# Kernel optimization log

Measured on AMD Instinct MI355X. Metric: run time of the kernel, lower is better.

Reference implementation:

```python
import jax, jax.numpy as jnp
import numpy as np
import math

B, N, D = 4, 2048, 256
H = 8
HD = D // H  # 32
EPS = 1e-5


def _layernorm(x, gamma, beta):
    mu = jnp.mean(x, axis=-1, keepdims=True)
    var = jnp.var(x, axis=-1, keepdims=True)
    return (x - mu) * jax.lax.rsqrt(var + EPS) * gamma + beta


def setup_inputs() -> dict:
    key = jax.random.key(0)
    ks = jax.random.split(key, 16)
    s = 0.02
    inp = {
        "x": jax.random.normal(ks[0], (B, N, D), dtype=jnp.float32),
        "adj": jax.random.randint(ks[1], (B, N, N), 0, 2, dtype=jnp.int32),
        "wq": jax.random.normal(ks[2], (D, D), dtype=jnp.float32) * s,
        "bq": jnp.zeros((D,), jnp.float32),
        "wk": jax.random.normal(ks[3], (D, D), dtype=jnp.float32) * s,
        "bk": jnp.zeros((D,), jnp.float32),
        "wv": jax.random.normal(ks[4], (D, D), dtype=jnp.float32) * s,
        "bv": jnp.zeros((D,), jnp.float32),
        "wo": jax.random.normal(ks[5], (D, D), dtype=jnp.float32) * s,
        "bo": jnp.zeros((D,), jnp.float32),
        "g1": jnp.ones((D,), jnp.float32),
        "be1": jnp.zeros((D,), jnp.float32),
        "g2": jnp.ones((D,), jnp.float32),
        "be2": jnp.zeros((D,), jnp.float32),
        "w1": jax.random.normal(ks[6], (D, 4 * D), dtype=jnp.float32) * s,
        "b1": jnp.zeros((4 * D,), jnp.float32),
        "w2": jax.random.normal(ks[7], (4 * D, D), dtype=jnp.float32) * s,
        "b2": jnp.zeros((D,), jnp.float32),
    }
    return inp


def reference(x, adj, wq, bq, wk, bk, wv, bv, wo, bo, g1, be1, g2, be2, w1, b1, w2, b2):
    # Dropout is identity in eval mode.
    res = x
    xn = _layernorm(x, g1, be1)
    q = (xn @ wq + bq).reshape(B, N, H, HD).transpose(0, 2, 1, 3)  # (B,H,N,d)
    k = (xn @ wk + bk).reshape(B, N, H, HD).transpose(0, 2, 1, 3)
    v = (xn @ wv + bv).reshape(B, N, H, HD).transpose(0, 2, 1, 3)
    scores = jnp.einsum("bhnd,bhmd->bhnm", q, k) / math.sqrt(HD)
    scores = jnp.where(adj[:, None, :, :] == 0, -jnp.inf, scores)
    attn = jax.nn.softmax(scores, axis=-1)
    attn = jnp.nan_to_num(attn, nan=0.0)  # rows with no edges -> all zeros
    out = jnp.einsum("bhnm,bhmd->bhnd", attn, v)
    out = out.transpose(0, 2, 1, 3).reshape(B, N, D)
    out = out @ wo + bo
    x = res + out
    h = _layernorm(x, g2, be2)
    h = jax.nn.gelu(h @ w1 + b1, approximate=False) @ w2 + b2
    return x + h
```

## Files before the change

### kernel.cpp

```cpp
#include <hip/hip_runtime.h>
#include <hip/hip_bf16.h>
#include <math.h>

#define B_ 4
#define N_ 2048
#define D_ 256
#define H_ 8
#define HD_ 32
#define F_ 1024
#define M_ (B_*N_)
#define EPS_ 1e-5f
#define VSTR 72

typedef __attribute__((ext_vector_type(8))) short short8;
typedef __attribute__((ext_vector_type(4))) float f32x4;

#define QSC 0.2550565499f

#if __has_builtin(__builtin_amdgcn_exp2f)
__device__ inline float fexp2(float x) { return __builtin_amdgcn_exp2f(x); }
#else
__device__ inline float fexp2(float x) { float r; asm("v_exp_f32 %0, %1" : "=v"(r) : "v"(x)); return r; }
#endif
#if __has_builtin(__builtin_amdgcn_rcpf)
__device__ inline float frcp(float x) { return __builtin_amdgcn_rcpf(x); }
#else
__device__ inline float frcp(float x) { float r; asm("v_rcp_f32 %0, %1" : "=v"(r) : "v"(x)); return r; }
#endif

__device__ inline unsigned short f2bf(float f) {
    union { float f; unsigned u; } x; x.f = f;
    unsigned r = x.u + 0x7fff + ((x.u >> 16) & 1);
    return (unsigned short)(r >> 16);
}

__device__ inline unsigned pk_bf16(float a, float b) {
    union { __hip_bfloat162 h; unsigned u; } c;
    c.h = __float22bfloat162_rn(float2{a, b});
    return c.u;
}

__device__ inline float gelu_f(float x) {
    float ax = fabsf(x);
    float z = ax * 0.70710678118654752f;
    float t = frcp(fmaf(0.3275911f, z, 1.0f));
    float e = fexp2(-z * z * 1.4426950408889634f);
    float poly = t * fmaf(t, fmaf(t, fmaf(t, fmaf(t, 1.061405429f, -1.453152027f),
                     1.421413741f), -0.284496736f), 0.254829592f);
    float erfv = 1.0f - poly * e;
    float s = (x < 0.f) ? -erfv : erfv;
    return 0.5f * x * (1.0f + s);
}

__device__ inline void async_copy16(const void* g, void* l) {
    __builtin_amdgcn_global_load_lds(
        (const __attribute__((address_space(1))) void*)g,
        (__attribute__((address_space(3))) void*)l, 16, 0, 0);
}

__device__ inline void ln_rows(const float* __restrict__ x,
        const float* __restrict__ g, const float* __restrict__ be,
        unsigned short* __restrict__ out, int blk) {
    int w = threadIdx.x >> 6, lane = threadIdx.x & 63;
    int row = blk * 4 + w;
    float4 v = *(const float4*)&x[(size_t)row * D_ + lane * 4];
    float s  = v.x + v.y + v.z + v.w;
    float s2 = v.x * v.x + v.y * v.y + v.z * v.z + v.w * v.w;
    #pragma unroll
    for (int off = 1; off < 64; off <<= 1) {
        s  += __shfl_xor(s,  off, 64);
        s2 += __shfl_xor(s2, off, 64);
    }
    float mu  = s * (1.0f / D_);
    float var = s2 * (1.0f / D_) - mu * mu;
    float r = rsqrtf(var + EPS_);
    float4 gv = *(const float4*)&g[lane * 4];
    float4 bv = *(const float4*)&be[lane * 4];
    ushort4 u;
    u.x = f2bf((v.x - mu) * r * gv.x + bv.x);
    u.y = f2bf((v.y - mu) * r * gv.y + bv.y);
    u.z = f2bf((v.z - mu) * r * gv.z + bv.z);
    u.w = f2bf((v.w - mu) * r * gv.w + bv.w);
    *(ushort4*)&out[(size_t)row * D_ + lane * 4] = u;
}

__global__ __launch_bounds__(256) void ln_kernel(const float* __restrict__ x,
        const float* __restrict__ g, const float* __restrict__ be,
        unsigned short* __restrict__ out) {
    ln_rows(x, g, be, out, blockIdx.x);
}

__global__ __launch_bounds__(256) void prep_kernel(
        const int* __restrict__ adj, unsigned short* __restrict__ mask16,
        const float* __restrict__ wq, const float* __restrict__ wk,
        const float* __restrict__ wv, const float* __restrict__ wo,
        const float* __restrict__ w1, const float* __restrict__ w2,
        unsigned short* __restrict__ wqkvt, unsigned short* __restrict__ wot,
        unsigned short* __restrict__ w1t, unsigned short* __restrict__ w2t,
        const float* __restrict__ x, const float* __restrict__ g1,
        const float* __restrict__ be1, unsigned short* __restrict__ xn) {
    __shared__ float t[32][33];
    int id = blockIdx.x;
    if (id < 4096) {
        int g = id * 256 + threadIdx.x;
        const int4* ap = (const int4*)adj + (size_t)g * 4;
        unsigned bits = 0;
        #pragma unroll
        for (int i = 0; i < 4; i++) {
            int4 v = ap[i];
            bits |= (v.x != 0 ? 1u : 0u) << (4 * i + 0);
            bits |= (v.y != 0 ? 1u : 0u) << (4 * i + 1);
            bits |= (v.z != 0 ? 1u : 0u) << (4 * i + 2);
            bits |= (v.w != 0 ? 1u : 0u) << (4 * i + 3);
        }
        mask16[g] = (unsigned short)bits;
        return;
    }
    if (id >= 4864) {
        ln_rows(x, g1, be1, xn, id - 4864);
        return;
    }
    id -= 4096;
    const float* W; unsigned short* Wt; int K, Nc, n0, k0;
    if (id < 256) {
        int m = id >> 6, l = id & 63;
        K = 256; Nc = 256; n0 = (l & 7) * 32; k0 = (l >> 3) * 32;
        W  = m == 0 ? wq : (m == 1 ? wk : (m == 2 ? wv : wo));
        Wt = m == 0 ? wqkvt : (m == 1 ? wqkvt + 65536 : (m == 2 ? wqkvt + 131072 : wot));
    } else if (id < 512) {
        int l = id - 256; K = 256; Nc = 1024; n0 = (l & 31) * 32; k0 = (l >> 5) * 32;
        W = w1; Wt = w1t;
    } else {
        int l = id - 512; K = 1024; Nc = 256; n0 = (l & 7) * 32; k0 = (l >> 3) * 32;
        W = w2; Wt = w2t;
    }
    int tx = threadIdx.x & 31, ty = threadIdx.x >> 5;
    #pragma unroll
    for (int i = 0; i < 4; i++)
        t[ty + i * 8][tx] = W[(size_t)(k0 + ty + i * 8) * Nc + n0 + tx];
    __syncthreads();
    #pragma unroll
    for (int i = 0; i < 4; i++)
        Wt[(size_t)(n0 + ty + i * 8) * K + k0 + tx] = f2bf(t[tx][ty + i * 8]);
}

#define GM_HEAD 0
#define GM_RES  1
#define GM_GELU 2

template<int MODE, int MI, int NI>
__global__ __launch_bounds__(256) void gemm_mfma(
        const unsigned short* __restrict__ A,
        const unsigned short* __restrict__ Bt,
        const float* __restrict__ bias, const float* __restrict__ bias2,
        const float* __restrict__ bias3, const float* __restrict__ res,
        void* __restrict__ Cout,
        unsigned short* __restrict__ q_out, unsigned short* __restrict__ k_out,
        unsigned short* __restrict__ v_out, int M, int Nc, int K) {
    constexpr int BM = MI * 32, BN = NI * 32;
    __shared__ __align__(16) unsigned short Abuf[2][BM * 32];
    __shared__ __align__(16) unsigned short Bbuf[2][BN * 32];
    int tid = threadIdx.x, w = tid >> 6, lane = tid & 63;
    int lr = lane & 15, lg = lane >> 4;
    int wy = w >> 1, wx = w & 1;
    int m0 = blockIdx.y * BM, n0 = blockIdx.x * BN;
    f32x4 acc[MI][NI] = {};

    int srow = lane >> 2;
    int schunk = lane & 3;

    auto STAGE = [&](int k0, int bi) {
        #pragma unroll
        for (int i = 0; i < BM / 64; i++) {
            int ar = i * 64 + w * 16 + srow;
            int ac = schunk ^ ((ar >> 1) & 3);
            async_copy16(A + (size_t)(m0 + ar) * K + k0 + ac * 8,
                         &Abuf[bi][(i * 64 + w * 16) * 32]);
        }
        #pragma unroll
        for (int i = 0; i < BN / 64; i++) {
            int br = i * 64 + w * 16 + srow;
            int bc = schunk ^ ((br >> 1) & 3);
            async_copy16(Bt + (size_t)(n0 + br) * K + k0 + bc * 8,
                         &Bbuf[bi][(i * 64 + w * 16) * 32]);
        }
    };

    int nkt = K / 32;
    STAGE(0, 0);
    for (int kt = 0; kt < nkt; kt++) {
        __syncthreads();
        int cur = kt & 1;
        if (kt + 1 < nkt) STAGE((kt + 1) * 32, cur ^ 1);

        short8 af[MI], bf[NI];
        #pragma unroll
        for (int mi = 0; mi < MI; mi++) {
            int r = wy * (MI * 16) + mi * 16 + lr;
            int c = lg ^ ((r >> 1) & 3);
            af[mi] = *(const short8*)&Abuf[cur][r * 32 + c * 8];
        }
        #pragma unroll
        for (int ni = 0; ni < NI; ni++) {
            int r = wx * (NI * 16) + ni * 16 + lr;
            int c = lg ^ ((r >> 1) & 3);
            bf[ni] = *(const short8*)&Bbuf[cur][r * 32 + c * 8];
        }
        #pragma unroll
        for (int mi = 0; mi < MI; mi++)
            #pragma unroll
            for (int ni = 0; ni < NI; ni++)
                acc[mi][ni] = __builtin_amdgcn_mfma_f32_16x16x32_bf16(
                        af[mi], bf[ni], acc[mi][ni], 0, 0, 0);
    }

    #pragma unroll
    for (int mi = 0; mi < MI; mi++) {
        #pragma unroll
        for (int r = 0; r < 4; r++) {
            int grow = m0 + wy * (MI * 16) + mi * 16 + lg * 4 + r;
            #pragma unroll
            for (int ni = 0; ni < NI; ni++) {
                int gcol = n0 + wx * (NI * 16) + ni * 16 + lr;
                float val = acc[mi][ni][r];
                if (MODE == GM_HEAD) {
                    int which = gcol >> 8, nn = gcol & 255;
                    const float* bp = which == 0 ? bias : (which == 1 ? bias2 : bias3);
                    val += bp[nn];
                    if (which == 0) val *= QSC;
                    unsigned short* dst = which == 0 ? q_out : (which == 1 ? k_out : v_out);
                    int bb = grow >> 11, rr = grow & (N_ - 1);
                    int hh = nn >> 5, dd = nn & 31;
                    dst[((((size_t)bb * H_ + hh) * N_) + rr) * HD_ + dd] = f2bf(val);
                } else if (MODE == GM_RES) {
                    val += bias[gcol] + res[(size_t)grow * Nc + gcol];
                    ((float*)Cout)[(size_t)grow * Nc + gcol] = val;
                } else {
                    val = gelu_f(val + bias[gcol]);
                    ((unsigned short*)Cout)[(size_t)grow * Nc + gcol] = f2bf(val);
                }
            }
        }
    }
}

__global__ __launch_bounds__(256) void attn_mfma7(
        const unsigned short* __restrict__ q, const unsigned short* __restrict__ k,
        const unsigned short* __restrict__ v, const unsigned long long* __restrict__ mask,
        unsigned short* __restrict__ ao) {
    __shared__ __align__(16) unsigned short Kb[2][64 * 32];
    __shared__ __align__(16) unsigned short Vt[2][32 * VSTR];
    int b = blockIdx.z, h = blockIdx.y;
    int q0 = blockIdx.x * 64;
    int tid = threadIdx.x, w = tid >> 6, lane = tid & 63;
    int lr = lane & 15, lg = lane >> 4;
    size_t bh = (size_t)(b * H_ + h);
    const unsigned short* qbp = q + bh * N_ * HD_;
    const unsigned short* kbp = k + bh * N_ * HD_;
    const unsigned short* vbp = v + bh * N_ * HD_;

    short8 qf = *(const short8*)&qbp[(size_t)(q0 + w * 16 + lr) * HD_ + lg * 8];
    const unsigned long long* mrow = mask + ((size_t)b * N_ + q0 + w * 16 + lr) * (N_ / 64);

    int swz = (lr & 3) ^ ((lr >> 2) & 3);
    int sr = lane >> 2, sc = lane & 3;
    int ssw = (sr & 3) ^ ((sr >> 2) & 3);
    const unsigned short* ksrc = kbp + (size_t)(w * 16 + sr) * HD_ + (sc ^ ssw) * 8;
    int va = tid & 31, vd = tid >> 5;
    const unsigned short* vsrc = vbp + (size_t)(2 * va) * HD_ + vd * 4;
    int p2 = 2 * va;
    int sig = (p2 & 35) | ((p2 & 12) << 1) | ((p2 & 16) >> 2);

    f32x4 acc0 = {}, acc1 = {};
    f32x4 zero = {};
    float l0a = 0.f, l1a = 0.f;
    const int NT = N_ / 64;

    {
        ushort4 v0p = *(const ushort4*)vsrc;
        ushort4 v1p = *(const ushort4*)(vsrc + HD_);
        async_copy16(ksrc, &Kb[0][w * 16 * 32]);
        *(unsigned*)&Vt[0][(vd * 4 + 0) * VSTR + sig] = ((unsigned)v1p.x << 16) | v0p.x;
        *(unsigned*)&Vt[0][(vd * 4 + 1) * VSTR + sig] = ((unsigned)v1p.y << 16) | v0p.y;
        *(unsigned*)&Vt[0][(vd * 4 + 2) * VSTR + sig] = ((unsigned)v1p.z << 16) | v0p.z;
        *(unsigned*)&Vt[0][(vd * 4 + 3) * VSTR + sig] = ((unsigned)v1p.w << 16) | v0p.w;
    }
    unsigned long long mk_cur = mrow[0], mk_next = 0;
    ushort4 v0n = {}, v1n = {};

    for (int t = 0; t < NT; t++) {
        __syncthreads();
        int cur = t & 1;
        if (t + 1 < NT) {
            size_t koff = (size_t)(t + 1) * 64 * HD_;
            v0n = *(const ushort4*)(vsrc + koff);
            v1n = *(const ushort4*)(vsrc + koff + HD_);
            async_copy16(ksrc + koff, &Kb[cur ^ 1][w * 16 * 32]);
            mk_next = mrow[t + 1];
        }

        f32x4 s[4];
        #pragma unroll
        for (int j = 0; j < 4; j++) {
            short8 kf = *(const short8*)&Kb[cur][(j * 16 + lr) * 32 + ((lg ^ swz) * 8)];
            s[j] = __builtin_amdgcn_mfma_f32_16x16x32_bf16(kf, qf, zero, 0, 0, 0);
        }

        unsigned mlo = (unsigned)(mk_cur >> (lg * 4));
        unsigned mhi = (unsigned)(mk_cur >> (lg * 4 + 32));
        #pragma unroll
        for (int j = 0; j < 4; j++) {
            unsigned mw = (j & 2) ? mhi : mlo;
            #pragma unroll
            for (int r = 0; r < 4; r++) {
                float sv = ((mw >> ((j & 1) * 16 + r)) & 1) ? s[j][r] : -200.f;
                float pv = fexp2(sv);
                s[j][r] = pv;
                if (j < 2) l0a += pv; else l1a += pv;
            }
        }

        union { short8 v8; unsigned u[4]; } pf0, pf1;
        pf0.u[0] = pk_bf16(s[0][0], s[0][1]); pf0.u[1] = pk_bf16(s[0][2], s[0][3]);
        pf0.u[2] = pk_bf16(s[1][0], s[1][1]); pf0.u[3] = pk_bf16(s[1][2], s[1][3]);
        pf1.u[0] = pk_bf16(s[2][0], s[2][1]); pf1.u[1] = pk_bf16(s[2][2], s[2][3]);
        pf1.u[2] = pk_bf16(s[3][0], s[3][1]); pf1.u[3] = pk_bf16(s[3][2], s[3][3]);

        short8 vfA0 = *(const short8*)&Vt[cur][lr * VSTR + lg * 8];
        short8 vfB0 = *(const short8*)&Vt[cur][(lr + 16) * VSTR + lg * 8];
        short8 vfA1 = *(const short8*)&Vt[cur][lr * VSTR + 32 + lg * 8];
        short8 vfB1 = *(const short8*)&Vt[cur][(lr + 16) * VSTR + 32 + lg * 8];
        acc0 = __builtin_amdgcn_mfma_f32_16x16x32_bf16(pf0.v8, vfA0, acc0, 0, 0, 0);
        acc1 = __builtin_amdgcn_mfma_f32_16x16x32_bf16(pf0.v8, vfB0, acc1, 0, 0, 0);
        acc0 = __builtin_amdgcn_mfma_f32_16x16x32_bf16(pf1.v8, vfA1, acc0, 0, 0, 0);
        acc1 = __builtin_amdgcn_mfma_f32_16x16x32_bf16(pf1.v8, vfB1, acc1, 0, 0, 0);

        if (t + 1 < NT) {
            *(unsigned*)&Vt[cur ^ 1][(vd * 4 + 0) * VSTR + sig] = ((unsigned)v1n.x << 16) | v0n.x;
            *(unsigned*)&Vt[cur ^ 1][(vd * 4 + 1) * VSTR + sig] = ((unsigned)v1n.y << 16) | v0n.y;
            *(unsigned*)&Vt[cur ^ 1][(vd * 4 + 2) * VSTR + sig] = ((unsigned)v1n.z << 16) | v0n.z;
            *(unsigned*)&Vt[cur ^ 1][(vd * 4 + 3) * VSTR + sig] = ((unsigned)v1n.w << 16) | v0n.w;
        }
        mk_cur = mk_next;
    }

    float l = l0a + l1a;
    l += __shfl_xor(l, 16, 64);
    l += __shfl_xor(l, 32, 64);
    float linv = (l > 0.f) ? 1.0f / l : 0.f;
    #pragma unroll
    for (int r = 0; r < 4; r++) {
        float ir = __shfl(linv, lg * 4 + r, 64);
        int row = q0 + w * 16 + lg * 4 + r;
        unsigned short* op = ao + ((size_t)(b * N_) + row) * D_ + h * HD_;
        op[lr]      = f2bf(acc0[r] * ir);
        op[lr + 16] = f2bf(acc1[r] * ir);
    }
}

extern "C" void kernel_launch(void* const* d_in, const int* in_sizes, int n_in,
                              void* d_out, int out_size, void* d_ws, size_t ws_size,
                              hipStream_t stream) {
    const float* x   = (const float*)d_in[0];
    const int*   adj = (const int*)d_in[1];
    const float* wq  = (const float*)d_in[2];
    const float* bq  = (const float*)d_in[3];
    const float* wk  = (const float*)d_in[4];
    const float* bk  = (const float*)d_in[5];
    const float* wv  = (const float*)d_in[6];
    const float* bv  = (const float*)d_in[7];
    const float* wo  = (const float*)d_in[8];
    const float* bo  = (const float*)d_in[9];
    const float* g1  = (const float*)d_in[10];
    const float* be1 = (const float*)d_in[11];
    const float* g2  = (const float*)d_in[12];
    const float* be2 = (const float*)d_in[13];
    const float* w1  = (const float*)d_in[14];
    const float* b1  = (const float*)d_in[15];
    const float* w2  = (const float*)d_in[16];
    const float* b2  = (const float*)d_in[17];
    float* out = (float*)d_out;
    char* base = (char*)d_ws;

    const size_t MB = (size_t)1 << 20;
    unsigned long long* mask = (unsigned long long*)(base);
    unsigned short* xn     = (unsigned short*)(base + 2*MB);
    unsigned short* qb     = (unsigned short*)(base + 6*MB);
    unsigned short* kb     = (unsigned short*)(base + 10*MB);
    unsigned short* vb     = (unsigned short*)(base + 14*MB);
    unsigned short* ao     = (unsigned short*)(base + 18*MB);
    float*          x2     = (float*)(base + 22*MB);
    unsigned short* hn     = (unsigned short*)(base + 30*MB);
    unsigned short* h1     = (unsigned short*)(base + 34*MB);
    unsigned short* wqkvt  = (unsigned short*)(base + 51*MB);
    unsigned short* wot    = (unsigned short*)(base + 51*MB + 394240);
    unsigned short* w1t    = (unsigned short*)(base + 52*MB);
    unsigned short* w2t    = (unsigned short*)(base + 52*MB + 524288);

    prep_kernel<<<4096 + 768 + 2048, 256, 0, stream>>>(
        adj, (unsigned short*)mask, wq, wk, wv, wo, w1, w2,
        wqkvt, wot, w1t, w2t, x, g1, be1, xn);
    gemm_mfma<GM_HEAD, 4, 2><<<dim3(12, 64), 256, 0, stream>>>(
        xn, wqkvt, bq, bk, bv, nullptr, nullptr, qb, kb, vb, M_, 768, 256);
    attn_mfma7<<<dim3(N_ / 64, H_, B_), 256, 0, stream>>>(qb, kb, vb, mask, ao);
    gemm_mfma<GM_RES, 4, 2><<<dim3(4, 64), 256, 0, stream>>>(
        ao, wot, bo, nullptr, nullptr, x, x2, nullptr, nullptr, nullptr, M_, 256, 256);
    ln_kernel<<<M_ / 4, 256, 0, stream>>>(x2, g2, be2, hn);
    gemm_mfma<GM_GELU, 4, 2><<<dim3(16, 64), 256, 0, stream>>>(
        hn, w1t, b1, nullptr, nullptr, nullptr, h1, nullptr, nullptr, nullptr, M_, 1024, 256);
    gemm_mfma<GM_RES, 4, 2><<<dim3(4, 64), 256, 0, stream>>>(
        h1, w2t, b2, nullptr, nullptr, x2, out, nullptr, nullptr, nullptr, M_, 256, 1024);
}
```

Measured before the change: 129.7 us.

## Make attention waves independent with register-prefetched K/V and MFMA row sums

The attention kernel drops the block-shared K tile and the per-iteration __syncthreads. Each wave now loads its K fragments straight from global memory into registers and keeps its own private transposed V buffer in LDS. Loads for the next tile are software-pipelined through two register sets, with the loop unrolled by two. The softmax denominator is now accumulated by an extra MFMA against a vector of ones instead of scalar adds plus cross-lane shuffles, and launch bounds request 4 blocks per SM. The trade-off is four times the global K/V traffic per block (mostly absorbed by cache) and higher register pressure, in exchange for no block-level barriers.

```diff
diff --git a/kernel.cpp b/kernel.cpp
--- a/kernel.cpp
+++ b/kernel.cpp
@@ -244,12 +244,11 @@
     }
 }
 
-__global__ __launch_bounds__(256) void attn_mfma7(
+__global__ __launch_bounds__(256, 4) void attn_mfma8(
         const unsigned short* __restrict__ q, const unsigned short* __restrict__ k,
         const unsigned short* __restrict__ v, const unsigned long long* __restrict__ mask,
         unsigned short* __restrict__ ao) {
-    __shared__ __align__(16) unsigned short Kb[2][64 * 32];
-    __shared__ __align__(16) unsigned short Vt[2][32 * VSTR];
+    __shared__ __align__(16) unsigned short Vt[4][32 * VSTR];
     int b = blockIdx.z, h = blockIdx.y;
     int q0 = blockIdx.x * 64;
     int tid = threadIdx.x, w = tid >> 6, lane = tid & 63;
@@ -262,95 +261,102 @@
     short8 qf = *(const short8*)&qbp[(size_t)(q0 + w * 16 + lr) * HD_ + lg * 8];
     const unsigned long long* mrow = mask + ((size_t)b * N_ + q0 + w * 16 + lr) * (N_ / 64);
 
-    int swz = (lr & 3) ^ ((lr >> 2) & 3);
-    int sr = lane >> 2, sc = lane & 3;
-    int ssw = (sr & 3) ^ ((sr >> 2) & 3);
-    const unsigned short* ksrc = kbp + (size_t)(w * 16 + sr) * HD_ + (sc ^ ssw) * 8;
-    int va = tid & 31, vd = tid >> 5;
-    const unsigned short* vsrc = vbp + (size_t)(2 * va) * HD_ + vd * 4;
+    const unsigned short* kfr = kbp + (size_t)lr * HD_ + lg * 8;
+    int va = lane & 31, dh = lane >> 5;
+    int d0 = dh * 16;
+    const unsigned short* vr0p = vbp + (size_t)(2 * va) * HD_ + d0;
+    const unsigned short* vr1p = vbp + (size_t)(2 * va + 1) * HD_ + d0;
     int p2 = 2 * va;
     int sig = (p2 & 35) | ((p2 & 12) << 1) | ((p2 & 16) >> 2);
-
-    f32x4 acc0 = {}, acc1 = {};
+    unsigned short* vt = &Vt[w][0];
+
+    short8 ones;
+    #pragma unroll
+    for (int i = 0; i < 8; i++) ones[i] = (short)0x3F80;
+
+    f32x4 acc0 = {}, acc1 = {}, acc_l = {};
     f32x4 zero = {};
-    float l0a = 0.f, l1a = 0.f;
     const int NT = N_ / 64;
 
-    {
-        ushort4 v0p = *(const ushort4*)vsrc;
-        ushort4 v1p = *(const ushort4*)(vsrc + HD_);
-        async_copy16(ksrc, &Kb[0][w * 16 * 32]);
-        *(unsigned*)&Vt[0][(vd * 4 + 0) * VSTR + sig] = ((unsigned)v1p.x << 16) | v0p.x;
-        *(unsigned*)&Vt[0][(vd * 4 + 1) * VSTR + sig] = ((unsigned)v1p.y << 16) | v0p.y;
-        *(unsigned*)&Vt[0][(vd * 4 + 2) * VSTR + sig] = ((unsigned)v1p.z << 16) | v0p.z;
-        *(unsigned*)&Vt[0][(vd * 4 + 3) * VSTR + sig] = ((unsigned)v1p.w << 16) | v0p.w;
-    }
-    unsigned long long mk_cur = mrow[0], mk_next = 0;
-    ushort4 v0n = {}, v1n = {};
-
-    for (int t = 0; t < NT; t++) {
-        __syncthreads();
-        int cur = t & 1;
-        if (t + 1 < NT) {
-            size_t koff = (size_t)(t + 1) * 64 * HD_;
-            v0n = *(const ushort4*)(vsrc + koff);
-            v1n = *(const ushort4*)(vsrc + koff + HD_);
-            async_copy16(ksrc + koff, &Kb[cur ^ 1][w * 16 * 32]);
-            mk_next = mrow[t + 1];
-        }
-
+    short8 kfA[4], kfB[4];
+    short8 vA0, vA1, vB0, vB1;
+    short8 vA2, vB2;
+    unsigned long long mkA, mkB;
+
+    #pragma unroll
+    for (int j = 0; j < 4; j++)
+        kfA[j] = *(const short8*)(kfr + (size_t)j * 16 * HD_);
+    vA0 = *(const short8*)vr0p;
+    vA1 = *(const short8*)(vr0p + 8);
+    vA2 = *(const short8*)vr1p;
+    short8 vA3 = *(const short8*)(vr1p + 8);
+    mkA = mrow[0];
+
+    auto TILE = [&](int t, short8* kfC, short8& c0, short8& c1, short8& c2, short8& c3,
+                    unsigned long long mkC,
+                    short8* kfN, short8& n0v, short8& n1v, short8& n2v, short8& n3v,
+                    unsigned long long& mkN) {
+        #pragma unroll
+        for (int dd = 0; dd < 8; dd++) {
+            unsigned pr0 = ((unsigned)(unsigned short)c2[dd] << 16) | (unsigned short)c0[dd];
+            *(unsigned*)&vt[(d0 + dd) * VSTR + sig] = pr0;
+            unsigned pr1 = ((unsigned)(unsigned short)c3[dd] << 16) | (unsigned short)c1[dd];
+            *(unsigned*)&vt[(d0 + 8 + dd) * VSTR + sig] = pr1;
+        }
         f32x4 s[4];
         #pragma unroll
-        for (int j = 0; j < 4; j++) {
-            short8 kf = *(const short8*)&Kb[cur][(j * 16 + lr) * 32 + ((lg ^ swz) * 8)];
-            s[j] = __builtin_amdgcn_mfma_f32_16x16x32_bf16(kf, qf, zero, 0, 0, 0);
-        }
-
-        unsigned mlo = (unsigned)(mk_cur >> (lg * 4));
-        unsigned mhi = (unsigned)(mk_cur >> (lg * 4 + 32));
+        for (int j = 0; j < 4; j++)
+            s[j] = __builtin_amdgcn_mfma_f32_16x16x32_bf16(kfC[j], qf, zero, 0, 0, 0);
+        int tn = (t + 1 < NT) ? (t + 1) : (NT - 1);
+        size_t koff = (size_t)tn * 64 * HD_;
+        #pragma unroll
+        for (int j = 0; j < 4; j++)
+            kfN[j] = *(const short8*)(kfr + koff + (size_t)j * 16 * HD_);
+        n0v = *(const short8*)(vr0p + koff);
+        n1v = *(const short8*)(vr0p + koff + 8);
+        n2v = *(const short8*)(vr1p + koff);
+        n3v = *(const short8*)(vr1p + koff + 8);
+        mkN = mrow[tn];
+        unsigned mlo = (unsigned)(mkC >> (lg * 4));
+        unsigned mhi = (unsigned)(mkC >> (lg * 4 + 32));
         #pragma unroll
         for (int j = 0; j < 4; j++) {
             unsigned mw = (j & 2) ? mhi : mlo;
             #pragma unroll
             for (int r = 0; r < 4; r++) {
                 float sv = ((mw >> ((j & 1) * 16 + r)) & 1) ? s[j][r] : -200.f;
-                float pv = fexp2(sv);
-                s[j][r] = pv;
-                if (j < 2) l0a += pv; else l1a += pv;
+                s[j][r] = fexp2(sv);
             }
         }
-
         union { short8 v8; unsigned u[4]; } pf0, pf1;
         pf0.u[0] = pk_bf16(s[0][0], s[0][1]); pf0.u[1] = pk_bf16(s[0][2], s[0][3]);
         pf0.u[2] = pk_bf16(s[1][0], s[1][1]); pf0.u[3] = pk_bf16(s[1][2], s[1][3]);
         pf1.u[0] = pk_bf16(s[2][0], s[2][1]); pf1.u[1] = pk_bf16(s[2][2], s[2][3]);
         pf1.u[2] = pk_bf16(s[3][0], s[3][1]); pf1.u[3] = pk_bf16(s[3][2], s[3][3]);
 
-        short8 vfA0 = *(const short8*)&Vt[cur][lr * VSTR + lg * 8];
-        short8 vfB0 = *(const short8*)&Vt[cur][(lr + 16) * VSTR + lg * 8];
-        short8 vfA1 = *(const short8*)&Vt[cur][lr * VSTR + 32 + lg * 8];
-        short8 vfB1 = *(const short8*)&Vt[cur][(lr + 16) * VSTR + 32 + lg * 8];
+        short8 vfA0 = *(const short8*)&vt[lr * VSTR + lg * 8];
+        short8 vfB0 = *(const short8*)&vt[(lr + 16) * VSTR + lg * 8];
+        short8 vfA1 = *(const short8*)&vt[lr * VSTR + 32 + lg * 8];
+        short8 vfB1 = *(const short8*)&vt[(lr + 16) * VSTR + 32 + lg * 8];
         acc0 = __builtin_amdgcn_mfma_f32_16x16x32_bf16(pf0.v8, vfA0, acc0, 0, 0, 0);
         acc1 = __builtin_amdgcn_mfma_f32_16x16x32_bf16(pf0.v8, vfB0, acc1, 0, 0, 0);
+        acc_l = __builtin_amdgcn_mfma_f32_16x16x32_bf16(pf0.v8, ones, acc_l, 0, 0, 0);
         acc0 = __builtin_amdgcn_mfma_f32_16x16x32_bf16(pf1.v8, vfA1, acc0, 0, 0, 0);
         acc1 = __builtin_amdgcn_mfma_f32_16x16x32_bf16(pf1.v8, vfB1, acc1, 0, 0, 0);
-
-        if (t + 1 < NT) {
-            *(unsigned*)&Vt[cur ^ 1][(vd * 4 + 0) * VSTR + sig] = ((unsigned)v1n.x << 16) | v0n.x;
-            *(unsigned*)&Vt[cur ^ 1][(vd * 4 + 1) * VSTR + sig] = ((unsigned)v1n.y << 16) | v0n.y;
-            *(unsigned*)&Vt[cur ^ 1][(vd * 4 + 2) * VSTR + sig] = ((unsigned)v1n.z << 16) | v0n.z;
-            *(unsigned*)&Vt[cur ^ 1][(vd * 4 + 3) * VSTR + sig] = ((unsigned)v1n.w << 16) | v0n.w;
-        }
-        mk_cur = mk_next;
-    }
-
-    float l = l0a + l1a;
-    l += __shfl_xor(l, 16, 64);
-    l += __shfl_xor(l, 32, 64);
-    float linv = (l > 0.f) ? 1.0f / l : 0.f;
+        acc_l = __builtin_amdgcn_mfma_f32_16x16x32_bf16(pf1.v8, ones, acc_l, 0, 0, 0);
+    };
+
+    #pragma unroll 1
+    for (int t = 0; t < NT; t += 2) {
+        TILE(t,     kfA, vA0, vA1, vA2, vA3, mkA, kfB, vB0, vB1, vB2, vA3, mkB);
+        short8 vB3 = vA3;
+        TILE(t + 1, kfB, vB0, vB1, vB2, vB3, mkB, kfA, vA0, vA1, vA2, vA3, mkA);
+    }
+
     #pragma unroll
     for (int r = 0; r < 4; r++) {
-        float ir = __shfl(linv, lg * 4 + r, 64);
+        float lv = acc_l[r];
+        float ir = (lv > 0.f) ? frcp(lv) : 0.f;
         int row = q0 + w * 16 + lg * 4 + r;
         unsigned short* op = ao + ((size_t)(b * N_) + row) * D_ + h * HD_;
         op[lr]      = f2bf(acc0[r] * ir);
@@ -402,7 +408,7 @@
         wqkvt, wot, w1t, w2t, x, g1, be1, xn);
     gemm_mfma<GM_HEAD, 4, 2><<<dim3(12, 64), 256, 0, stream>>>(
         xn, wqkvt, bq, bk, bv, nullptr, nullptr, qb, kb, vb, M_, 768, 256);
-    attn_mfma7<<<dim3(N_ / 64, H_, B_), 256, 0, stream>>>(qb, kb, vb, mask, ao);
+    attn_mfma8<<<dim3(N_ / 64, H_, B_), 256, 0, stream>>>(qb, kb, vb, mask, ao);
     gemm_mfma<GM_RES, 4, 2><<<dim3(4, 64), 256, 0, stream>>>(
         ao, wot, bo, nullptr, nullptr, x, x2, nullptr, nullptr, nullptr, M_, 256, 256);
     ln_kernel<<<M_ / 4, 256, 0, stream>>>(x2, g2, be2, hn);
```

After: 179.3 us. +38.2%, slower.
